# Kernel optimization log

Hardware: AMD Instinct MI355X
Metric: run time of the kernel (lower is better)

Reference implementation:

```python
import jax, jax.numpy as jnp
import numpy as np

N, D_IN, D_H, D_OUT = 100000, 40, 30, 10
B, NN, R = 10000, 64, 10
EPS = 1e-5          # kernel_eps
LENGTH_SCALE = 1.0  # Matern length scale
# nu = 0.5 -> Matern-1/2 kernel: K(d) = exp(-d / length_scale)


def setup_inputs() -> dict:
    key = jax.random.key(0)
    ks = jax.random.split(key, 8)
    x = jax.random.normal(ks[0], (N, D_IN), jnp.float32)
    batch_indices = jax.random.randint(ks[1], (B,), 0, N)
    batch_nn_indices = jax.random.randint(ks[2], (B, NN), 0, N)
    batch_targets = jax.random.normal(ks[3], (B, R), jnp.float32)
    batch_nn_targets = jax.random.normal(ks[4], (B, NN, R), jnp.float32)
    W1 = jax.random.normal(ks[5], (D_H, D_IN), jnp.float32) / np.sqrt(D_IN).astype(np.float32)
    b1 = jnp.zeros((D_H,), jnp.float32)
    a1 = jnp.float32(0.25)  # PReLU(1) slope
    W2 = jax.random.normal(ks[6], (D_OUT, D_H), jnp.float32) / np.sqrt(D_H).astype(np.float32)
    b2 = jnp.zeros((D_OUT,), jnp.float32)
    a2 = jnp.float32(0.25)
    return dict(x=x, batch_indices=batch_indices, batch_nn_indices=batch_nn_indices,
                batch_targets=batch_targets, batch_nn_targets=batch_nn_targets,
                W1=W1, b1=b1, a1=a1, W2=W2, b2=b2, a2=a2)


def _prelu(x, a):
    return jnp.where(x > 0, x, a * x)


def _matern_half(d):
    return jnp.exp(-d / LENGTH_SCALE)


def reference(x, batch_indices, batch_nn_indices, batch_targets, batch_nn_targets,
              W1, b1, a1, W2, b2, a2):
    # --- embedding MLP (eval mode: dropout = identity) ---
    h = _prelu(x @ W1.T + b1, a1)
    emb = _prelu(h @ W2.T + b2, a2)            # [N, D_OUT]

    # --- gather neighborhoods ---
    xb = emb[batch_indices]                     # [B, d]
    xnn = emb[batch_nn_indices]                 # [B, nn, d]

    # --- crosswise / pairwise l2 distances (via squared-norm expansion) ---
    sq_b = jnp.sum(xb * xb, axis=-1)            # [B]
    sq_nn = jnp.sum(xnn * xnn, axis=-1)         # [B, nn]
    d2_cross = sq_b[:, None] + sq_nn - 2.0 * jnp.einsum('bd,bnd->bn', xb, xnn)
    d_cross = jnp.sqrt(jnp.maximum(d2_cross, 0.0))                    # [B, nn]
    d2_pair = sq_nn[:, :, None] + sq_nn[:, None, :] \
        - 2.0 * jnp.einsum('bnd,bmd->bnm', xnn, xnn)
    d_pair = jnp.sqrt(jnp.maximum(d2_pair, 0.0))                      # [B, nn, nn]

    Kcross = _matern_half(d_cross)              # [B, nn]
    K = _matern_half(d_pair)                    # [B, nn, nn]
    Kplus = K + EPS * jnp.eye(NN, dtype=K.dtype)

    # single batched solve with concatenated RHS [targets | Kcross]
    rhs = jnp.concatenate([batch_nn_targets, Kcross[..., None]], axis=-1)  # [B, nn, R+1]
    sol = jnp.linalg.solve(Kplus, rhs)
    coeffs = sol[..., :R]                       # (K+eI)^-1 Y    [B, nn, R]
    kc_solve = sol[..., R]                      # (K+eI)^-1 k*   [B, nn]

    predictions = jnp.einsum('bn,bnr->br', Kcross, coeffs)                # [B, R]
    variances = 1.0 - jnp.einsum('bn,bn->b', Kcross, kc_solve)            # [B]
    sigma_sq = jnp.einsum('bnr,bnr->r', batch_nn_targets, coeffs) / (B * NN)  # [R]
    return predictions, variances, sigma_sq
```

## Files before the change

kernel.cpp:

```cpp
#include <hip/hip_runtime.h>
#include <cstdint>

#define N_PTS 100000
#define DIN   40
#define DH    30
#define DOUT  10
#define NB    10000
#define NNB   64
#define NR    10
#define EPSF  1e-5f

__device__ __forceinline__ float rcp_nr(float x) {
    float r = __builtin_amdgcn_rcpf(x);
    return r * (2.0f - x * r);
}

__device__ __forceinline__ float fast_sqrt(float x) {
    return __builtin_amdgcn_sqrtf(x);
}

__device__ __forceinline__ float lane_bcast(float x, int lane) {
    return __int_as_float(__builtin_amdgcn_readlane(__float_as_int(x), lane));
}

__device__ __forceinline__ void fma_arch(float& a, const float negm, const float p) {
    asm("v_fmac_f32 %0, %2, %1" : "+v"(a) : "v"(negm), "s"(p));
}

__global__ __launch_bounds__(256) void mlp_kernel(
    const float* __restrict__ x,
    const float* __restrict__ W1, const float* __restrict__ b1, const float* __restrict__ a1p,
    const float* __restrict__ W2, const float* __restrict__ b2, const float* __restrict__ a2p,
    float* __restrict__ emb)
{
    __shared__ float sW1[DH * DIN];
    __shared__ float sW2[DOUT * DH];
    __shared__ float sb1[DH];
    __shared__ float sb2[DOUT];
    for (int i = threadIdx.x; i < DH * DIN; i += 256) sW1[i] = W1[i];
    for (int i = threadIdx.x; i < DOUT * DH; i += 256) sW2[i] = W2[i];
    if (threadIdx.x < DH)   sb1[threadIdx.x] = b1[threadIdx.x];
    if (threadIdx.x < DOUT) sb2[threadIdx.x] = b2[threadIdx.x];
    const float a1 = a1p[0], a2 = a2p[0];
    __syncthreads();

    const int n = blockIdx.x * 256 + threadIdx.x;
    if (n >= N_PTS) return;

    float xv[DIN];
    const float4* xp = reinterpret_cast<const float4*>(x + (size_t)n * DIN);
#pragma unroll
    for (int q = 0; q < DIN / 4; ++q) {
        float4 v = xp[q];
        xv[4*q+0] = v.x; xv[4*q+1] = v.y; xv[4*q+2] = v.z; xv[4*q+3] = v.w;
    }

    float h[DH];
#pragma unroll
    for (int i = 0; i < DH; ++i) {
        float acc = sb1[i];
#pragma unroll
        for (int j = 0; j < DIN; ++j) acc = fmaf(xv[j], sW1[i * DIN + j], acc);
        h[i] = acc > 0.0f ? acc : a1 * acc;
    }

    float* eo = emb + (size_t)n * DOUT;
#pragma unroll
    for (int d = 0; d < DOUT; ++d) {
        float acc = sb2[d];
#pragma unroll
        for (int i = 0; i < DH; ++i) acc = fmaf(h[i], sW2[d * DH + i], acc);
        eo[d] = acc > 0.0f ? acc : a2 * acc;
    }
}


template<int J>
struct Build {
    static __device__ __forceinline__ void run(float (&ar)[NNB], const float (&xn)[DOUT],
                                               const float sq, const int lane) {
        float px[DOUT];
#pragma unroll
        for (int d = 0; d < DOUT; ++d) px[d] = lane_bcast(xn[d], J);
        float dj = 0.0f;
#pragma unroll
        for (int d = 0; d < DOUT; ++d) dj = fmaf(px[d], xn[d], dj);
        const float sqj = lane_bcast(sq, J);
        const float d2  = sq + sqj - 2.0f * dj;
        const float kij = __expf(-fast_sqrt(fmaxf(d2, 0.0f)));
        ar[J] = (J == lane) ? (1.0f + EPSF) : kij;
        Build<J + 1>::run(ar, xn, sq, lane);
    }
};
template<>
struct Build<NNB> {
    static __device__ __forceinline__ void run(float (&)[NNB], const float (&)[DOUT],
                                               float, int) {}
};

template<int K, int J, int CNT>
struct Grp {
    static __device__ __forceinline__ void run(float (&ar)[NNB], const float negm) {
        float p[CNT];
#pragma unroll
        for (int t = 0; t < CNT; ++t) p[t] = lane_bcast(ar[J + t], K);
#pragma unroll
        for (int t = 0; t < CNT; ++t) fma_arch(ar[J + t], negm, p[t]);
    }
};

template<int K, int J>
struct Suffix {
    static __device__ __forceinline__ void run(float (&ar)[NNB], const float negm) {
        constexpr int REM = NNB - J;
        constexpr int CNT = (REM < 8) ? REM : 8;
        Grp<K, J, CNT>::run(ar, negm);
        if constexpr (J + CNT < NNB) Suffix<K, J + CNT>::run(ar, negm);
    }
};

template<int K>
struct GJ {
    static __device__ __forceinline__ void run(float (&ar)[NNB], float (&rr)[NR + 1],
                                               float& mydiag, const int lane,
                                               const float inv) {
        const float m    = (lane == K) ? 0.0f : ar[K] * inv;
        const float negm = -m;
        mydiag = (lane == K) ? ar[K] : mydiag;

        {
            const float p = lane_bcast(ar[K + 1], K);
            fma_arch(ar[K + 1], negm, p);
        }
        const float inv_next = rcp_nr(lane_bcast(ar[K + 1], K + 1));

        if constexpr (K + 2 < NNB) Suffix<K, K + 2>::run(ar, negm);

        {
            float pr[NR + 1];
#pragma unroll
            for (int r = 0; r <= NR; ++r) pr[r] = lane_bcast(rr[r], K);
#pragma unroll
            for (int r = 0; r <= NR; ++r) fma_arch(rr[r], negm, pr[r]);
        }

        GJ<K + 1>::run(ar, rr, mydiag, lane, inv_next);
    }
};
template<>
struct GJ<NNB - 1> {
    static __device__ __forceinline__ void run(float (&ar)[NNB], float (&rr)[NR + 1],
                                               float& mydiag, const int lane,
                                               const float inv) {
        constexpr int K  = NNB - 1;
        const float m    = (lane == K) ? 0.0f : ar[K] * inv;
        const float negm = -m;
        mydiag = (lane == K) ? ar[K] : mydiag;
        float pr[NR + 1];
#pragma unroll
        for (int r = 0; r <= NR; ++r) pr[r] = lane_bcast(rr[r], K);
#pragma unroll
        for (int r = 0; r <= NR; ++r) fma_arch(rr[r], negm, pr[r]);
    }
};

__global__ __launch_bounds__(128, 2) void solve_kernel(
    const float* __restrict__ emb,
    const int* __restrict__ bidx,
    const int* __restrict__ bnn,
    const float* __restrict__ tnn_g,
    float* __restrict__ pred,
    float* __restrict__ var,
    float* __restrict__ part)
{
    const int wave = threadIdx.x >> 6;
    const int lane = threadIdx.x & 63;
    const int b    = blockIdx.x * 2 + wave;

    const int idx = bnn[b * NNB + lane];
    float xn[DOUT];
    {
        const float2* ep = reinterpret_cast<const float2*>(emb + (size_t)idx * DOUT);
#pragma unroll
        for (int q = 0; q < DOUT / 2; ++q) { float2 v = ep[q]; xn[2*q] = v.x; xn[2*q+1] = v.y; }
    }
    const int bi = bidx[b];
    float sq = 0.0f, dotb = 0.0f, sqb = 0.0f;
#pragma unroll
    for (int d = 0; d < DOUT; ++d) {
        const float xbd = emb[(size_t)bi * DOUT + d];
        sq   = fmaf(xn[d], xn[d], sq);
        dotb = fmaf(xbd, xn[d], dotb);
        sqb  = fmaf(xbd, xbd, sqb);
    }
    const float d2c = sqb + sq - 2.0f * dotb;
    const float kc  = __expf(-fast_sqrt(fmaxf(d2c, 0.0f)));

    float ar[NNB];
    Build<0>::run(ar, xn, sq, lane);

    float rr[NR + 1];
    {
        const float2* tp = reinterpret_cast<const float2*>(
            tnn_g + (size_t)b * NNB * NR + (size_t)lane * NR);
#pragma unroll
        for (int q = 0; q < NR / 2; ++q) { float2 v = tp[q]; rr[2*q] = v.x; rr[2*q+1] = v.y; }
    }
    rr[NR] = kc;

    const float inv0 = rcp_nr(lane_bcast(ar[0], 0));
    float mydiag = 1.0f;
    GJ<0>::run(ar, rr, mydiag, lane, inv0);
    const float dinv = rcp_nr(mydiag);

    float tn[NR];
    {
        const float2* tp = reinterpret_cast<const float2*>(
            tnn_g + (size_t)b * NNB * NR + (size_t)lane * NR);
#pragma unroll
        for (int q = 0; q < NR / 2; ++q) { float2 v = tp[q]; tn[2*q] = v.x; tn[2*q+1] = v.y; }
    }

    float pv[NR], sg[NR];
#pragma unroll
    for (int r = 0; r < NR; ++r) {
        const float xr = rr[r] * dinv;
        pv[r] = kc * xr;
        sg[r] = tn[r] * xr;
    }
    float vv = kc * rr[NR] * dinv;
#pragma unroll
    for (int off = 32; off > 0; off >>= 1) {
#pragma unroll
        for (int r = 0; r < NR; ++r) {
            pv[r] += __shfl_xor(pv[r], off);
            sg[r] += __shfl_xor(sg[r], off);
        }
        vv += __shfl_xor(vv, off);
    }
    if (lane == 0) {
#pragma unroll
        for (int r = 0; r < NR; ++r) {
            pred[b * NR + r] = pv[r];
            part[b * NR + r] = sg[r];
        }
        var[b] = 1.0f - vv;
    }
}

__global__ __launch_bounds__(256) void reduce_kernel(
    const float* __restrict__ part, float* __restrict__ sig)
{
    float acc[NR];
#pragma unroll
    for (int r = 0; r < NR; ++r) acc[r] = 0.0f;
    for (int b = threadIdx.x; b < NB; b += 256) {
#pragma unroll
        for (int r = 0; r < NR; ++r) acc[r] += part[b * NR + r];
    }
#pragma unroll
    for (int off = 32; off > 0; off >>= 1) {
#pragma unroll
        for (int r = 0; r < NR; ++r) acc[r] += __shfl_xor(acc[r], off);
    }
    __shared__ float s[4][NR];
    const int w = threadIdx.x >> 6, l = threadIdx.x & 63;
    if (l == 0) {
#pragma unroll
        for (int r = 0; r < NR; ++r) s[w][r] = acc[r];
    }
    __syncthreads();
    if (threadIdx.x == 0) {
        const float scale = 1.0f / ((float)NB * (float)NNB);
#pragma unroll
        for (int r = 0; r < NR; ++r)
            sig[r] = (s[0][r] + s[1][r] + s[2][r] + s[3][r]) * scale;
    }
}

extern "C" void kernel_launch(void* const* d_in, const int* in_sizes, int n_in,
                              void* d_out, int out_size, void* d_ws, size_t ws_size,
                              hipStream_t stream)
{
    const float* x    = (const float*)d_in[0];
    const int*   bidx = (const int*)  d_in[1];
    const int*   bnn  = (const int*)  d_in[2];
    const float* tnn  = (const float*)d_in[4];
    const float* W1   = (const float*)d_in[5];
    const float* b1   = (const float*)d_in[6];
    const float* a1   = (const float*)d_in[7];
    const float* W2   = (const float*)d_in[8];
    const float* b2   = (const float*)d_in[9];
    const float* a2   = (const float*)d_in[10];

    float* out  = (float*)d_out;
    float* pred = out;
    float* var  = out + NB * NR;
    float* sig  = out + NB * NR + NB;

    float* emb  = (float*)d_ws;
    float* part = emb + (size_t)N_PTS * DOUT;

    mlp_kernel<<<(N_PTS + 255) / 256, 256, 0, stream>>>(x, W1, b1, a1, W2, b2, a2, emb);
    solve_kernel<<<NB / 2, 128, 0, stream>>>(emb, bidx, bnn, tnn, pred, var, part);
    reduce_kernel<<<1, 256, 0, stream>>>(part, sig);
}
```

Before: 187.4 us.

## Replace Gauss-Jordan elimination with forward elimination plus back-substitution

Replaces full Gauss-Jordan elimination with Gaussian forward elimination (only rows below the pivot are updated) followed by a lane-serial back-substitution over the right-hand sides. The matrix updates still run over the whole register row, but the backward pass only touches the 11 RHS columns, trading some elimination work for a serial dependency chain of 64 steps with readlane broadcasts. It also moves from two waves per 128-thread block to one wave per 64-thread block with launch bounds (64,1), which changes register budget and occupancy.

```diff
diff --git a/kernel.cpp b/kernel.cpp
--- a/kernel.cpp
+++ b/kernel.cpp
@@ -120,13 +120,11 @@
 };
 
 template<int K>
-struct GJ {
+struct Fwd {
     static __device__ __forceinline__ void run(float (&ar)[NNB], float (&rr)[NR + 1],
-                                               float& mydiag, const int lane,
-                                               const float inv) {
-        const float m    = (lane == K) ? 0.0f : ar[K] * inv;
+                                               const int lane, const float inv) {
+        const float m    = (lane > K) ? ar[K] * inv : 0.0f;
         const float negm = -m;
-        mydiag = (lane == K) ? ar[K] : mydiag;
 
         {
             const float p = lane_bcast(ar[K + 1], K);
@@ -144,27 +142,36 @@
             for (int r = 0; r <= NR; ++r) fma_arch(rr[r], negm, pr[r]);
         }
 
-        GJ<K + 1>::run(ar, rr, mydiag, lane, inv_next);
+        Fwd<K + 1>::run(ar, rr, lane, inv_next);
     }
 };
 template<>
-struct GJ<NNB - 1> {
+struct Fwd<NNB - 1> {
+    static __device__ __forceinline__ void run(float (&)[NNB], float (&)[NR + 1],
+                                               int, float) {}
+};
+
+template<int K>
+struct Bwd {
     static __device__ __forceinline__ void run(float (&ar)[NNB], float (&rr)[NR + 1],
-                                               float& mydiag, const int lane,
-                                               const float inv) {
-        constexpr int K  = NNB - 1;
-        const float m    = (lane == K) ? 0.0f : ar[K] * inv;
-        const float negm = -m;
-        mydiag = (lane == K) ? ar[K] : mydiag;
-        float pr[NR + 1];
-#pragma unroll
-        for (int r = 0; r <= NR; ++r) pr[r] = lane_bcast(rr[r], K);
-#pragma unroll
-        for (int r = 0; r <= NR; ++r) fma_arch(rr[r], negm, pr[r]);
-    }
-};
-
-__global__ __launch_bounds__(128, 2) void solve_kernel(
+                                               const int lane, const float invd) {
+        const float m = (lane < K) ? ar[K] : 0.0f;
+        float xk[NR + 1];
+#pragma unroll
+        for (int r = 0; r <= NR; ++r) xk[r] = lane_bcast(rr[r], K) * invd;
+
+        float invd_next = 0.0f;
+        if constexpr (K > 0) invd_next = rcp_nr(lane_bcast(ar[K - 1], K - 1));
+
+#pragma unroll
+        for (int r = 0; r <= NR; ++r)
+            rr[r] = (lane == K) ? xk[r] : fmaf(-m, xk[r], rr[r]);
+
+        if constexpr (K > 0) Bwd<K - 1>::run(ar, rr, lane, invd_next);
+    }
+};
+
+__global__ __launch_bounds__(64, 1) void solve_kernel(
     const float* __restrict__ emb,
     const int* __restrict__ bidx,
     const int* __restrict__ bnn,
@@ -173,9 +180,8 @@
     float* __restrict__ var,
     float* __restrict__ part)
 {
-    const int wave = threadIdx.x >> 6;
-    const int lane = threadIdx.x & 63;
-    const int b    = blockIdx.x * 2 + wave;
+    const int lane = threadIdx.x;
+    const int b    = blockIdx.x;
 
     const int idx = bnn[b * NNB + lane];
     float xn[DOUT];
@@ -209,9 +215,10 @@
     rr[NR] = kc;
 
     const float inv0 = rcp_nr(lane_bcast(ar[0], 0));
-    float mydiag = 1.0f;
-    GJ<0>::run(ar, rr, mydiag, lane, inv0);
-    const float dinv = rcp_nr(mydiag);
+    Fwd<0>::run(ar, rr, lane, inv0);
+
+    const float invd63 = rcp_nr(lane_bcast(ar[NNB - 1], NNB - 1));
+    Bwd<NNB - 1>::run(ar, rr, lane, invd63);
 
     float tn[NR];
     {
@@ -223,12 +230,8 @@
 
     float pv[NR], sg[NR];
 #pragma unroll
-    for (int r = 0; r < NR; ++r) {
-        const float xr = rr[r] * dinv;
-        pv[r] = kc * xr;
-        sg[r] = tn[r] * xr;
-    }
-    float vv = kc * rr[NR] * dinv;
+    for (int r = 0; r < NR; ++r) { pv[r] = kc * rr[r]; sg[r] = tn[r] * rr[r]; }
+    float vv = kc * rr[NR];
 #pragma unroll
     for (int off = 32; off > 0; off >>= 1) {
 #pragma unroll
@@ -302,6 +305,6 @@
     float* part = emb + (size_t)N_PTS * DOUT;
 
     mlp_kernel<<<(N_PTS + 255) / 256, 256, 0, stream>>>(x, W1, b1, a1, W2, b2, a2, emb);
-    solve_kernel<<<NB / 2, 128, 0, stream>>>(emb, bidx, bnn, tnn, pred, var, part);
+    solve_kernel<<<NB, 64, 0, stream>>>(emb, bidx, bnn, tnn, pred, var, part);
     reduce_kernel<<<1, 256, 0, stream>>>(part, sig);
 }
```

After: 334.7 us. 1.79x slower.
